# Optimization experiments

Measured on AMD Instinct MI355X. Metric: run time of the kernel, lower is better.

## Reference

```python
import jax, jax.numpy as jnp
import numpy as np

B, LQ, LK, H, DK, DV, E = 4, 1024, 1024, 12, 64, 768, 768
TOPK = 64
TEMP = 0.5
NEG = -10000.0


def setup_inputs() -> dict:
    key = jax.random.key(0)
    ks = jax.random.split(key, 10)
    s = 0.02  # weight init scale
    return {
        "q": jax.random.normal(ks[0], (B, LQ, E), jnp.float32),
        "k": jax.random.normal(ks[1], (B, LK, E), jnp.float32),
        "v": jax.random.normal(ks[2], (B, LK, DV), jnp.float32),
        "qpos": jnp.zeros((B, LQ), jnp.int32),
        "kpos": jnp.zeros((B, LK), jnp.int32),
        "qk_mask": jax.random.normal(ks[3], (B, 1, LQ, LK), jnp.float32) * 0.1,
        "k_mask": jax.random.normal(ks[4], (B, 1, LK, 1), jnp.float32) * 0.1,
        "post_softmax_mask": (jax.random.uniform(ks[5], (B, 1, LQ, LK)) > 0.1).astype(jnp.float32),
        "w_qs": jax.random.normal(ks[6], (E, H * DK), jnp.float32) * s,
        "w_ks": jax.random.normal(ks[7], (E, H * DK), jnp.float32) * s,
        "w_vs": jax.random.normal(ks[8], (DV, H * DV), jnp.float32) * s,
        "fc": jax.random.normal(ks[9], (H * DV, DV), jnp.float32) * s,
    }


def reference(q, k, v, qpos, kpos, qk_mask, k_mask, post_softmax_mask, w_qs, w_ks, w_vs, fc):
    residual = v
    # project and split heads: [b, len, h, d] -> [b, h, len, d]
    qh = (q @ w_qs).reshape(B, LQ, H, DK).transpose(0, 2, 1, 3)
    kh = (k @ w_ks).reshape(B, LK, H, DK).transpose(0, 2, 1, 3)
    vh = (v @ w_vs).reshape(B, LK, H, DV).transpose(0, 2, 1, 3)

    # scaled dot-product scores [b, h, lq, lk]
    attn = jnp.einsum('bhqd,bhkd->bhqk', qh / np.float32(np.sqrt(DK)), kh)
    attn = attn + qk_mask                              # additive qk mask
    attn = attn + jnp.squeeze(k_mask, -1)[:, :, None, :]  # additive key mask

    # topk sparsification: keep top-k scores, fill rest with -10000
    topk_vals, topk_idx = jax.lax.top_k(attn, TOPK)
    attn = jnp.put_along_axis(jnp.full_like(attn, NEG), topk_idx, topk_vals,
                              axis=-1, inplace=False)

    # temperature + stable softmax in fp32
    attn = attn / max(TEMP, 1e-6)
    attn = jax.nn.softmax(attn.astype(jnp.float32), axis=-1).astype(v.dtype)

    # post-softmax multiplicative mask + renorm (renorm_post_mask=True)
    attn = attn * post_softmax_mask
    attn = attn / jnp.maximum(attn.sum(axis=-1, keepdims=True), 1e-6)

    # straight-through argmax hardening (use_argmax=True)
    hard = jax.nn.one_hot(jnp.argmax(attn, axis=-1), LK, dtype=attn.dtype)
    attn = hard - jax.lax.stop_gradient(attn) + attn

    # attend, merge heads, output projection + residual (dropout=0)
    head_output = jnp.einsum('bhqk,bhkd->bhqd', attn, vh)
    output = head_output.transpose(0, 2, 1, 3).reshape(B, LQ, H * DV) @ fc
    output = output + residual
    return (output, attn)
```

## Files before the change

### kernel.cpp

```cpp
#include <hip/hip_runtime.h>

constexpr int NB  = 4;
constexpr int NH  = 12;
constexpr int SEQ = 1024;
constexpr int DKd = 64;
constexpr int DVd = 768;
constexpr int Ed  = 768;
constexpr int HVd = 9216;

typedef float f32x4 __attribute__((ext_vector_type(4)));
typedef short s16x8 __attribute__((ext_vector_type(8)));

__device__ __forceinline__ unsigned short f2bf(float f) {
  unsigned int u = __builtin_bit_cast(unsigned int, f);
  u += 0x7fffu + ((u >> 16) & 1u);
  return (unsigned short)(u >> 16);
}
__device__ __forceinline__ float bf2f(unsigned short h) {
  return __builtin_bit_cast(float, (unsigned int)h << 16);
}
__device__ __forceinline__ float bf2f_lo(unsigned int u) {
  return __builtin_bit_cast(float, u << 16);
}
__device__ __forceinline__ float bf2f_hi(unsigned int u) {
  return __builtin_bit_cast(float, u & 0xffff0000u);
}
__device__ __forceinline__ bool better(float va, int ia, float vb, int ib) {
  return va > vb || (va == vb && ia < ib);
}

__device__ __forceinline__ f32x4 mfma_bf16_16x16x32(s16x8 a, s16x8 b, f32x4 c) {
  asm("v_mfma_f32_16x16x32_bf16 %0, %1, %2, %0" : "+v"(c) : "v"(a), "v"(b));
  return c;
}

#define GLOAD16(g, l)                                                          \
  __builtin_amdgcn_global_load_lds(                                            \
      (const __attribute__((address_space(1))) unsigned int*)(g),              \
      (__attribute__((address_space(3))) unsigned int*)(l), 16, 0, 0)

__global__ __launch_bounds__(256)
void split_qk_kernel(const float* __restrict__ q, const float* __restrict__ k,
                     unsigned short* __restrict__ Qhi, unsigned short* __restrict__ Qlo,
                     unsigned short* __restrict__ Khi, unsigned short* __restrict__ Klo,
                     int n4) {
  const float* src = blockIdx.z ? k : q;
  unsigned short* hi = blockIdx.z ? Khi : Qhi;
  unsigned short* lo = blockIdx.z ? Klo : Qlo;
  int i = blockIdx.x * 256 + threadIdx.x;
  const int stride = gridDim.x * 256;
  for (; i < n4; i += stride) {
    const f32x4 x = *(const f32x4*)&src[(size_t)i * 4];
    unsigned short h[4], l[4];
#pragma unroll
    for (int c = 0; c < 4; c++) {
      h[c] = f2bf(x[c]);
      l[c] = f2bf(x[c] - bf2f(h[c]));
    }
    uint2 uh, ul;
    uh.x = (unsigned)h[0] | ((unsigned)h[1] << 16);
    uh.y = (unsigned)h[2] | ((unsigned)h[3] << 16);
    ul.x = (unsigned)l[0] | ((unsigned)l[1] << 16);
    ul.y = (unsigned)l[2] | ((unsigned)l[3] << 16);
    *(uint2*)&hi[(size_t)i * 4] = uh;
    *(uint2*)&lo[(size_t)i * 4] = ul;
  }
}

__global__ __launch_bounds__(256)
void split_wT_kernel(const float* __restrict__ w_qs, const float* __restrict__ w_ks,
                     unsigned short* __restrict__ WqThi, unsigned short* __restrict__ WqTlo,
                     unsigned short* __restrict__ WkThi, unsigned short* __restrict__ WkTlo) {
  __shared__ float Ts[64][68];
  const float* src = blockIdx.z ? w_ks : w_qs;
  unsigned short* hi = blockIdx.z ? WkThi : WqThi;
  unsigned short* lo = blockIdx.z ? WkTlo : WqTlo;
  const int e0 = blockIdx.x * 64, n0 = blockIdx.y * 64;
  const int tid = threadIdx.x;
  const int row = tid >> 2, cc = (tid & 3) * 16;
#pragma unroll
  for (int j = 0; j < 4; j++)
    *(f32x4*)&Ts[row][cc + 4 * j] = *(const f32x4*)&src[(size_t)(e0 + row) * 768 + n0 + cc + 4 * j];
  __syncthreads();
  const int r = tid >> 2, cs = (tid & 3) * 16;
  s16x8 ph[2], pl[2];
#pragma unroll
  for (int j = 0; j < 16; j++) {
    const float v = Ts[cs + j][r];
    const unsigned short h = f2bf(v);
    const unsigned short l = f2bf(v - bf2f(h));
    ph[j >> 3][j & 7] = (short)h;
    pl[j >> 3][j & 7] = (short)l;
  }
  const size_t ob = (size_t)(n0 + r) * 768 + e0 + cs;
  *(s16x8*)&hi[ob] = ph[0];
  *(s16x8*)&hi[ob + 8] = ph[1];
  *(s16x8*)&lo[ob] = pl[0];
  *(s16x8*)&lo[ob + 8] = pl[1];
}

__global__ __launch_bounds__(256)
void qkproj_mfma_kernel(const unsigned short* __restrict__ Qhi, const unsigned short* __restrict__ Qlo,
                        const unsigned short* __restrict__ Khi, const unsigned short* __restrict__ Klo,
                        const unsigned short* __restrict__ WqThi, const unsigned short* __restrict__ WqTlo,
                        const unsigned short* __restrict__ WkThi, const unsigned short* __restrict__ WkTlo,
                        float* __restrict__ qh, float* __restrict__ kh) {
  const unsigned short* Ahi = blockIdx.z ? Khi : Qhi;
  const unsigned short* Alo = blockIdx.z ? Klo : Qlo;
  const unsigned short* Bhi = blockIdx.z ? WkThi : WqThi;
  const unsigned short* Blo = blockIdx.z ? WkTlo : WqTlo;
  float* C = blockIdx.z ? kh : qh;
  __shared__ unsigned short AhiS[128 * 64], AloS[128 * 64];
  __shared__ unsigned short BhiS[64 * 64], BloS[64 * 64];
  const int tid = threadIdx.x;
  const int wid = tid >> 6, lane = tid & 63;
  const int m0 = blockIdx.x * 128, n0 = blockIdx.y * 64;
  const int wr = (wid >> 1) * 64, wc = (wid & 1) * 32;
  const int lm = lane & 15, lq = lane >> 4;
  const int srow = wid * 8 + (lane >> 3);
  const int scols = (((lane & 7) * 16) ^ ((srow & 7) << 4)) >> 1;
  const int ldst = wid * 512;
  const int xs = (lm & 7) << 3;

  const unsigned short* ahi0 = Ahi + (size_t)(m0 + srow) * 768 + scols;
  const unsigned short* alo0 = Alo + (size_t)(m0 + srow) * 768 + scols;
  const unsigned short* bhi0 = Bhi + (size_t)(n0 + srow) * 768 + scols;
  const unsigned short* blo0 = Blo + (size_t)(n0 + srow) * 768 + scols;

  f32x4 acc[4][2];
#pragma unroll
  for (int m = 0; m < 4; m++)
#pragma unroll
    for (int n = 0; n < 2; n++)
#pragma unroll
      for (int r = 0; r < 4; r++) acc[m][n][r] = 0.f;

  for (int k0 = 0; k0 < 768; k0 += 64) {
#pragma unroll
    for (int j = 0; j < 4; j++) {
      GLOAD16(ahi0 + (size_t)j * 32 * 768 + k0, &AhiS[j * 2048 + ldst]);
      GLOAD16(alo0 + (size_t)j * 32 * 768 + k0, &AloS[j * 2048 + ldst]);
    }
#pragma unroll
    for (int j = 0; j < 2; j++) {
      GLOAD16(bhi0 + (size_t)j * 32 * 768 + k0, &BhiS[j * 2048 + ldst]);
      GLOAD16(blo0 + (size_t)j * 32 * 768 + k0, &BloS[j * 2048 + ldst]);
    }
    __syncthreads();
#pragma unroll
    for (int ks = 0; ks < 2; ks++) {
      const int kc = (ks * 32 + lq * 8) ^ xs;
      s16x8 ah[4], al[4], bh[2], bl[2];
#pragma unroll
      for (int m = 0; m < 4; m++) {
        ah[m] = *(const s16x8*)&AhiS[(wr + m * 16 + lm) * 64 + kc];
        al[m] = *(const s16x8*)&AloS[(wr + m * 16 + lm) * 64 + kc];
      }
#pragma unroll
      for (int n = 0; n < 2; n++) {
        bh[n] = *(const s16x8*)&BhiS[(wc + n * 16 + lm) * 64 + kc];
        bl[n] = *(const s16x8*)&BloS[(wc + n * 16 + lm) * 64 + kc];
      }
#pragma unroll
      for (int m = 0; m < 4; m++)
#pragma unroll
        for (int n = 0; n < 2; n++) {
          acc[m][n] = mfma_bf16_16x16x32(ah[m], bh[n], acc[m][n]);
          acc[m][n] = mfma_bf16_16x16x32(al[m], bh[n], acc[m][n]);
          acc[m][n] = mfma_bf16_16x16x32(ah[m], bl[n], acc[m][n]);
        }
    }
    __syncthreads();
  }
  asm volatile("s_nop 7\n\ts_nop 7");
#pragma unroll
  for (int m = 0; m < 4; m++)
#pragma unroll
    for (int n = 0; n < 2; n++)
#pragma unroll
      for (int r = 0; r < 4; r++)
        C[(size_t)(m0 + wr + m * 16 + lq * 4 + r) * 768 + n0 + wc + n * 16 + lm] =
            acc[m][n][r];
}

__global__ __launch_bounds__(256)
void score_argmax_kernel(const float* __restrict__ qh, const float* __restrict__ kh,
                         const float* __restrict__ qkm, const float* __restrict__ km,
                         const float* __restrict__ pm, float4* __restrict__ partials) {
  __shared__ float msS[64][128];
  __shared__ float QsT[64][64];
  __shared__ float KsT[64][128];
  const int b  = blockIdx.z;
  const int q0 = blockIdx.y * 64;
  const int k0 = blockIdx.x * 128;
  const int tid = threadIdx.x;
  const int ty = tid >> 4, tx = tid & 15;

  {
    const int row = tid >> 2, cc = (tid & 3) * 32;
    const size_t base = (size_t)(b * SEQ + q0 + row) * SEQ + k0 + cc;
#pragma unroll
    for (int i = 0; i < 8; i++) {
      const f32x4 qv = *(const f32x4*)&qkm[base + 4 * i];
      const f32x4 pv = *(const f32x4*)&pm[base + 4 * i];
      const f32x4 kv = *(const f32x4*)&km[b * SEQ + k0 + cc + 4 * i];
      f32x4 o;
#pragma unroll
      for (int c = 0; c < 4; c++) o[c] = pv[c] > 0.f ? qv[c] + kv[c] : -3.0e38f;
      *(f32x4*)&msS[row][cc + 4 * i] = o;
    }
  }

  const int qr = tid >> 2, qdc = (tid & 3) * 16;
  const int kr = tid >> 1, kdc = (tid & 1) * 32;
  const float* qbase = qh + (size_t)(b * SEQ + q0 + qr) * Ed + qdc;
  const float* kbase = kh + (size_t)(b * SEQ + k0 + kr) * Ed + kdc;
  const int kg0 = k0 + tx * 8;

  for (int h = 0; h < NH; h++) {
    __syncthreads();
#pragma unroll
    for (int j = 0; j < 4; j++) {
      const f32x4 qv = *(const f32x4*)&qbase[h * 64 + 4 * j];
#pragma unroll
      for (int c = 0; c < 4; c++) QsT[qdc + 4 * j + c][qr] = qv[c];
    }
#pragma unroll
    for (int j = 0; j < 8; j++) {
      const f32x4 kv = *(const f32x4*)&kbase[h * 64 + 4 * j];
#pragma unroll
      for (int c = 0; c < 4; c++) KsT[kdc + 4 * j + c][kr] = kv[c];
    }
    __syncthreads();

    float acc[4][8];
#pragma unroll
    for (int i = 0; i < 4; i++)
#pragma unroll
      for (int j = 0; j < 8; j++) acc[i][j] = 0.f;

#pragma unroll 8
    for (int kk = 0; kk < 64; kk++) {
      const f32x4 qf  = *(const f32x4*)&QsT[kk][ty * 4];
      const f32x4 kf0 = *(const f32x4*)&KsT[kk][tx * 8];
      const f32x4 kf1 = *(const f32x4*)&KsT[kk][tx * 8 + 4];
#pragma unroll
      for (int i = 0; i < 4; i++)
#pragma unroll
        for (int j = 0; j < 4; j++) {
          acc[i][j]     += qf[i] * kf0[j];
          acc[i][j + 4] += qf[i] * kf1[j];
        }
    }

#pragma unroll
    for (int i = 0; i < 4; i++) {
      const int qg = q0 + ty * 4 + i;
      const f32x4 m0v = *(const f32x4*)&msS[ty * 4 + i][tx * 8];
      const f32x4 m1v = *(const f32x4*)&msS[ty * 4 + i][tx * 8 + 4];
      float v1 = -3.0e38f, v2 = -3.0e38f;
      int i1 = 0, i2 = 0;
#pragma unroll
      for (int j = 0; j < 8; j++) {
        const float s = acc[i][j] * 0.125f + (j < 4 ? m0v[j & 3] : m1v[j & 3]);
        const int idx = kg0 + j;
        if (better(s, idx, v1, i1)) { v2 = v1; i2 = i1; v1 = s; i1 = idx; }
        else if (better(s, idx, v2, i2)) { v2 = s; i2 = idx; }
      }
#pragma unroll
      for (int off = 1; off < 16; off <<= 1) {
        const float w1 = __shfl_xor(v1, off); const int j1 = __shfl_xor(i1, off);
        const float w2 = __shfl_xor(v2, off); const int j2 = __shfl_xor(i2, off);
        if (better(w1, j1, v1, i1)) {
          if (better(v1, i1, w2, j2)) { v2 = v1; i2 = i1; } else { v2 = w2; i2 = j2; }
          v1 = w1; i1 = j1;
        } else if (better(w1, j1, v2, i2)) { v2 = w1; i2 = j1; }
      }
      if (tx == 0)
        partials[(size_t)((b * NH + h) * SEQ + qg) * 8 + blockIdx.x] =
            make_float4(v1, __int_as_float(i1), v2, __int_as_float(i2));
    }
  }
}

__global__ __launch_bounds__(256)
void argmax_reduce_kernel(const float4* __restrict__ partials, int* __restrict__ kmaxp,
                          float4* __restrict__ aux) {
  const int t = blockIdx.x * 256 + threadIdx.x;
  if (t >= NB * NH * SEQ) return;
  const float4* p = partials + (size_t)t * 8;
  float v1 = -3.0e38f, v2 = -3.0e38f;
  int i1 = 0, i2 = 0;
#pragma unroll
  for (int i = 0; i < 8; i++) {
    const float w1 = p[i].x; const int j1 = __float_as_int(p[i].y);
    const float w2 = p[i].z; const int j2 = __float_as_int(p[i].w);
    if (better(w1, j1, v1, i1)) {
      if (better(v1, i1, w2, j2)) { v2 = v1; i2 = i1; } else { v2 = w2; i2 = j2; }
      v1 = w1; i1 = j1;
    } else if (better(w1, j1, v2, i2)) { v2 = w1; i2 = j1; }
  }
  kmaxp[t] = i1;
  aux[t] = make_float4(v1, __int_as_float(i1), v2, __int_as_float(i2));
}

__global__ __launch_bounds__(256)
void rescue_kernel(const float4* __restrict__ aux, const float* __restrict__ q,
                   const float* __restrict__ k, const float* __restrict__ w_qs,
                   const float* __restrict__ w_ks, const float* __restrict__ qkm,
                   const float* __restrict__ km, const float* __restrict__ pm,
                   int* __restrict__ kmaxp) {
  const int row = blockIdx.x * 4 + (threadIdx.x >> 6);
  const float4 a = aux[row];
  if (a.x - a.z > 5e-4f) return;
  const int i1 = __float_as_int(a.y), i2 = __float_as_int(a.w);
  if (i1 == i2) return;
  const int bh = row >> 10, qq = row & 1023;
  const int b = bh / NH, h = bh % NH;
  const int lane = threadIdx.x & 63;
  const float* qr = q + (size_t)(b * SEQ + qq) * Ed;
  const float* k1 = k + (size_t)(b * SEQ + i1) * Ed;
  const float* k2 = k + (size_t)(b * SEQ + i2) * Ed;
  const float* wq = w_qs + h * DKd + lane;
  const float* wk = w_ks + h * DKd + lane;
  float qd = 0.f, k1d = 0.f, k2d = 0.f;
#pragma unroll 4
  for (int e = 0; e < Ed; e++) {
    const float wqe = wq[(size_t)e * 768];
    const float wke = wk[(size_t)e * 768];
    qd  += qr[e] * wqe;
    k1d += k1[e] * wke;
    k2d += k2[e] * wke;
  }
  float s1 = qd * k1d, s2 = qd * k2d;
#pragma unroll
  for (int off = 1; off < 64; off <<= 1) {
    s1 += __shfl_xor(s1, off);
    s2 += __shfl_xor(s2, off);
  }
  const size_t m1 = (size_t)(b * SEQ + qq) * SEQ + i1;
  const size_t m2 = (size_t)(b * SEQ + qq) * SEQ + i2;
  s1 = s1 * 0.125f + (pm[m1] > 0.f ? qkm[m1] + km[b * SEQ + i1] : -3.0e38f);
  s2 = s2 * 0.125f + (pm[m2] > 0.f ? qkm[m2] + km[b * SEQ + i2] : -3.0e38f);
  if (lane == 0) kmaxp[row] = better(s1, i1, s2, i2) ? i1 : i2;
}

__global__ __launch_bounds__(256)
void cvt_bf16_kernel(const float* __restrict__ v, unsigned short* __restrict__ Vbf, int n4) {
  int i = blockIdx.x * 256 + threadIdx.x;
  const int stride = gridDim.x * 256;
  for (; i < n4; i += stride) {
    const f32x4 x = *(const f32x4*)&v[(size_t)i * 4];
    uint2 u;
    u.x = (unsigned)f2bf(x[0]) | ((unsigned)f2bf(x[1]) << 16);
    u.y = (unsigned)f2bf(x[2]) | ((unsigned)f2bf(x[3]) << 16);
    *(uint2*)&Vbf[(size_t)i * 4] = u;
  }
}

__global__ __launch_bounds__(256)
void wvfc_gemm_kernel(const float* __restrict__ wvs, const float* __restrict__ fcw,
                      unsigned short* __restrict__ MstbT) {
  __shared__ unsigned short As[128][72];
  __shared__ unsigned short Bs[128][72];
  const int tid = threadIdx.x;
  const int h = blockIdx.z;
  const int m0 = blockIdx.x * 128, n0 = blockIdx.y * 128;
  const int wid = tid >> 6, lane = tid & 63;
  const int wr = (wid >> 1) * 64, wc = (wid & 1) * 64;
  const int lm = lane & 15, lq = lane >> 4;
  const int ar = tid >> 1, acb = (tid & 1) * 32;
  const int br = tid >> 2, bnb = (tid & 3) * 32;

  f32x4 acc[4][4];
#pragma unroll
  for (int m = 0; m < 4; m++)
#pragma unroll
    for (int n = 0; n < 4; n++)
#pragma unroll
      for (int r = 0; r < 4; r++) acc[m][n][r] = 0.f;

  for (int k0 = 0; k0 < 768; k0 += 64) {
    const float* asrc = wvs + (size_t)(m0 + ar) * HVd + h * 768 + k0 + acb;
    const float* bsrc = fcw + (size_t)(h * 768 + k0 + br) * 768 + n0 + bnb;
    f32x4 a4[8], b4[8];
#pragma unroll
    for (int i = 0; i < 8; i++) a4[i] = *(const f32x4*)&asrc[4 * i];
#pragma unroll
    for (int i = 0; i < 8; i++) b4[i] = *(const f32x4*)&bsrc[4 * i];
    __syncthreads();
#pragma unroll
    for (int i = 0; i < 4; i++) {
      s16x8 pk;
#pragma unroll
      for (int j = 0; j < 8; j++) pk[j] = (short)f2bf(a4[2 * i + (j >> 2)][j & 3]);
      *(s16x8*)&As[ar][acb + 8 * i] = pk;
    }
#pragma unroll
    for (int i = 0; i < 8; i++)
#pragma unroll
      for (int c = 0; c < 4; c++) Bs[bnb + 4 * i + c][br] = f2bf(b4[i][c]);
    __syncthreads();
#pragma unroll
    for (int ks = 0; ks < 2; ks++) {
      s16x8 af[4], bfr[4];
#pragma unroll
      for (int m = 0; m < 4; m++)
        af[m] = *(const s16x8*)&As[wr + m * 16 + lm][ks * 32 + lq * 8];
#pragma unroll
      for (int n = 0; n < 4; n++)
        bfr[n] = *(const s16x8*)&Bs[wc + n * 16 + lm][ks * 32 + lq * 8];
#pragma unroll
      for (int m = 0; m < 4; m++)
#pragma unroll
        for (int n = 0; n < 4; n++)
          acc[m][n] = mfma_bf16_16x16x32(af[m], bfr[n], acc[m][n]);
    }
  }
  asm volatile("s_nop 7\n\ts_nop 7");
#pragma unroll
  for (int m = 0; m < 4; m++)
#pragma unroll
    for (int n = 0; n < 4; n++) {
      const int grow0 = m0 + wr + m * 16 + lq * 4;
      const int gcol  = n0 + wc + n * 16 + lm;
      uint2 u;
      u.x = (unsigned)f2bf(acc[m][n][0]) | ((unsigned)f2bf(acc[m][n][1]) << 16);
      u.y = (unsigned)f2bf(acc[m][n][2]) | ((unsigned)f2bf(acc[m][n][3]) << 16);
      *(uint2*)&MstbT[(size_t)(h * 768 + gcol) * 768 + grow0] = u;
    }
}

__global__ __launch_bounds__(256)
void ugemm_kernel(const unsigned short* __restrict__ Vbf,
                  const unsigned short* __restrict__ MstbT,
                  unsigned short* __restrict__ U, int h0) {
  __shared__ unsigned short As[128 * 64];
  __shared__ unsigned short Bs[128 * 64];
  const int tid = threadIdx.x;
  const int h = h0 + blockIdx.z;
  const int bx = (int)blockIdx.x;
  const int sx = ((bx & 7) << 2) | (bx >> 3);
  const int m0 = sx * 128, n0 = blockIdx.y * 128;
  const int wid = tid >> 6, lane = tid & 63;
  const int wr = (wid >> 1) * 64, wc = (wid & 1) * 64;
  const int lm = lane & 15, lq = lane >> 4;
  const int srow = tid >> 3, scol = (tid & 7) * 8;
  const int ldst = (tid >> 6) * 512;

  const unsigned short* asrc = Vbf + (size_t)(m0 + srow) * 768 + scol;
  const unsigned short* bsrc = MstbT + (size_t)(h * 768 + n0 + srow) * 768 + scol;

  f32x4 acc[4][4];
#pragma unroll
  for (int m = 0; m < 4; m++)
#pragma unroll
    for (int n = 0; n < 4; n++)
#pragma unroll
      for (int r = 0; r < 4; r++) acc[m][n][r] = 0.f;

  for (int k0 = 0; k0 < 768; k0 += 64) {
#pragma unroll
    for (int j = 0; j < 4; j++)
      GLOAD16(asrc + (size_t)j * 32 * 768 + k0, &As[j * 2048 + ldst]);
#pragma unroll
    for (int j = 0; j < 4; j++)
      GLOAD16(bsrc + (size_t)j * 32 * 768 + k0, &Bs[j * 2048 + ldst]);
    __syncthreads();
#pragma unroll
    for (int ks = 0; ks < 2; ks++) {
      s16x8 af[4], bfr[4];
#pragma unroll
      for (int m = 0; m < 4; m++)
        af[m] = *(const s16x8*)&As[(wr + m * 16 + lm) * 64 + ks * 32 + lq * 8];
#pragma unroll
      for (int n = 0; n < 4; n++)
        bfr[n] = *(const s16x8*)&Bs[(wc + n * 16 + lm) * 64 + ks * 32 + lq * 8];
#pragma unroll
      for (int m = 0; m < 4; m++)
#pragma unroll
        for (int n = 0; n < 4; n++)
          acc[m][n] = mfma_bf16_16x16x32(af[m], bfr[n], acc[m][n]);
    }
    __syncthreads();
  }
  asm volatile("s_nop 7\n\ts_nop 7");
  const size_t urow0 = (size_t)blockIdx.z * 4096;
#pragma unroll
  for (int m = 0; m < 4; m++)
#pragma unroll
    for (int r = 0; r < 4; r++) {
      const int row = m0 + wr + m * 16 + lq * 4 + r;
      uint2 u;
      u.x = (unsigned)f2bf(acc[m][0][r]) | ((unsigned)f2bf(acc[m][1][r]) << 16);
      u.y = (unsigned)f2bf(acc[m][2][r]) | ((unsigned)f2bf(acc[m][3][r]) << 16);
      *(uint2*)&U[(urow0 + row) * 768 + n0 + wc + lm * 4] = u;
    }
}

__global__ __launch_bounds__(192)
void gathersum_kernel(const unsigned short* __restrict__ U, const int* __restrict__ kmaxp,
                      const float* __restrict__ v, float* __restrict__ out0,
                      int h0, int nhg) {
  const int row = blockIdx.x;
  const int b = row >> 10, q = row & 1023;
  const int t = threadIdx.x;
  float a0 = 0.f, a1 = 0.f, a2 = 0.f, a3 = 0.f;
  for (int hg = 0; hg < nhg; hg++) {
    const int g = kmaxp[((b * NH + h0 + hg) << 10) + q];
    const uint2 u = *(const uint2*)&U[((size_t)hg * 4096 + (b << 10) + g) * 768 + t * 4];
    a0 += bf2f_lo(u.x);
    a1 += bf2f_hi(u.x);
    a2 += bf2f_lo(u.y);
    a3 += bf2f_hi(u.y);
  }
  const int chunk = t >> 4, lmm = t & 15;
  const size_t ob = (size_t)row * 768 + chunk * 64 + lmm;
  if (h0 == 0) {
    out0[ob +  0] = a0 + v[ob +  0];
    out0[ob + 16] = a1 + v[ob + 16];
    out0[ob + 32] = a2 + v[ob + 32];
    out0[ob + 48] = a3 + v[ob + 48];
  } else {
    out0[ob +  0] += a0;
    out0[ob + 16] += a1;
    out0[ob + 32] += a2;
    out0[ob + 48] += a3;
  }
}

__global__ void onehot_kernel(const int* __restrict__ kmaxp, f32x4* __restrict__ attn, int n4) {
  int i = blockIdx.x * blockDim.x + threadIdx.x;
  const int stride = gridDim.x * blockDim.x;
  for (; i < n4; i += stride) {
    const int row = i >> 8;
    const int c0 = (i & 255) * 4;
    const int km = kmaxp[row];
    f32x4 o;
#pragma unroll
    for (int c = 0; c < 4; c++) o[c] = (c0 + c == km) ? 1.0f : 0.0f;
    attn[i] = o;
  }
}

extern "C" void kernel_launch(void* const* d_in, const int* in_sizes, int n_in,
                              void* d_out, int out_size, void* d_ws, size_t ws_size,
                              hipStream_t stream) {
  (void)in_sizes; (void)n_in; (void)out_size;
  const float* q       = (const float*)d_in[0];
  const float* k       = (const float*)d_in[1];
  const float* v       = (const float*)d_in[2];
  const float* qk_mask = (const float*)d_in[5];
  const float* k_mask  = (const float*)d_in[6];
  const float* pmask   = (const float*)d_in[7];
  const float* w_qs    = (const float*)d_in[8];
  const float* w_ks    = (const float*)d_in[9];
  const float* w_vs    = (const float*)d_in[10];
  const float* fc      = (const float*)d_in[11];

  float* out0 = (float*)d_out;
  float* attn = out0 + (size_t)NB * SEQ * DVd;

  char* ws = (char*)d_ws;
  unsigned short* Qhi   = (unsigned short*)ws;
  unsigned short* Qlo   = (unsigned short*)(ws + 6291456);
  unsigned short* WqThi = (unsigned short*)(ws + 12582912);
  unsigned short* WqTlo = (unsigned short*)(ws + 13762560);
  unsigned short* WkThi = (unsigned short*)(ws + 14942208);
  unsigned short* WkTlo = (unsigned short*)(ws + 16121856);
  int* kmaxp            = (int*)(ws + 20447232);
  unsigned short* Khi   = (unsigned short*)(ws + 20643840);
  unsigned short* Klo   = (unsigned short*)(ws + 26935296);
  float* qh             = (float*)(ws + 33226752);
  float* kh             = (float*)(ws + 45809664);
  float4* partials      = (float4*)ws;
  float4* aux           = (float4*)(ws + 6291456);
  unsigned short* MstbT = (unsigned short*)ws;
  unsigned short* Vbf   = (unsigned short*)(ws + 14155776);
  unsigned short* U     = (unsigned short*)(ws + 20643840);

  const bool big = ws_size >= (size_t)96141312;

  split_qk_kernel<<<dim3(1536, 1, 2), 256, 0, stream>>>(q, k, Qhi, Qlo, Khi, Klo,
                                                        NB * SEQ * Ed / 4);
  split_wT_kernel<<<dim3(12, 12, 2), 256, 0, stream>>>(w_qs, w_ks, WqThi, WqTlo,
                                                       WkThi, WkTlo);

  qkproj_mfma_kernel<<<dim3(32, 12, 2), 256, 0, stream>>>(
      Qhi, Qlo, Khi, Klo, WqThi, WqTlo, WkThi, WkTlo, qh, kh);

  score_argmax_kernel<<<dim3(8, 16, NB), 256, 0, stream>>>(qh, kh, qk_mask, k_mask,
                                                           pmask, partials);
  argmax_reduce_kernel<<<dim3(192), 256, 0, stream>>>(partials, kmaxp, aux);

  rescue_kernel<<<dim3(12288), 256, 0, stream>>>(aux, q, k, w_qs, w_ks,
                                                 qk_mask, k_mask, pmask, kmaxp);

  cvt_bf16_kernel<<<dim3(3072), 256, 0, stream>>>(v, Vbf, NB * SEQ * DVd / 4);
  wvfc_gemm_kernel<<<dim3(6, 6, NH), 256, 0, stream>>>(w_vs, fc, MstbT);

  if (big) {
    ugemm_kernel<<<dim3(32, 6, 12), 256, 0, stream>>>(Vbf, MstbT, U, 0);
    gathersum_kernel<<<dim3(NB * SEQ), 192, 0, stream>>>(U, kmaxp, v, out0, 0, 12);
  } else {
    ugemm_kernel<<<dim3(32, 6, 6), 256, 0, stream>>>(Vbf, MstbT, U, 0);
    gathersum_kernel<<<dim3(NB * SEQ), 192, 0, stream>>>(U, kmaxp, v, out0, 0, 6);
    ugemm_kernel<<<dim3(32, 6, 6), 256, 0, stream>>>(Vbf, MstbT, U, 6);
    gathersum_kernel<<<dim3(NB * SEQ), 192, 0, stream>>>(U, kmaxp, v, out0, 6, 6);
  }

  onehot_kernel<<<dim3(2048), 256, 0, stream>>>(kmaxp, (f32x4*)attn,
                                                (int)((size_t)NB * NH * SEQ * SEQ / 4));
}
```

Baseline: 500.3 us.

## Compute attention scores with split-bf16 MFMA per head instead of FP32 FMA

```diff
diff --git a/kernel.cpp b/kernel.cpp
--- a/kernel.cpp
+++ b/kernel.cpp
@@ -184,88 +184,110 @@
 }
 
 __global__ __launch_bounds__(256)
-void score_argmax_kernel(const float* __restrict__ qh, const float* __restrict__ kh,
-                         const float* __restrict__ qkm, const float* __restrict__ km,
-                         const float* __restrict__ pm, float4* __restrict__ partials) {
-  __shared__ float msS[64][128];
-  __shared__ float QsT[64][64];
-  __shared__ float KsT[64][128];
-  const int b  = blockIdx.z;
-  const int q0 = blockIdx.y * 64;
-  const int k0 = blockIdx.x * 128;
+void score_mfma2_kernel(const float* __restrict__ qh, const float* __restrict__ kh,
+                        const float* __restrict__ qkm, const float* __restrict__ km,
+                        const float* __restrict__ pm, float4* __restrict__ partials) {
+  __shared__ unsigned short QhS[128][72], QlS[128][72];
+  __shared__ unsigned short KhS[128][72], KlS[128][72];
+  const int bh = blockIdx.z, b = bh / NH, h = bh % NH;
+  const int q0 = blockIdx.y * 128, k0 = blockIdx.x * 128;
   const int tid = threadIdx.x;
-  const int ty = tid >> 4, tx = tid & 15;
-
-  {
-    const int row = tid >> 2, cc = (tid & 3) * 32;
-    const size_t base = (size_t)(b * SEQ + q0 + row) * SEQ + k0 + cc;
-#pragma unroll
-    for (int i = 0; i < 8; i++) {
-      const f32x4 qv = *(const f32x4*)&qkm[base + 4 * i];
-      const f32x4 pv = *(const f32x4*)&pm[base + 4 * i];
-      const f32x4 kv = *(const f32x4*)&km[b * SEQ + k0 + cc + 4 * i];
-      f32x4 o;
-#pragma unroll
-      for (int c = 0; c < 4; c++) o[c] = pv[c] > 0.f ? qv[c] + kv[c] : -3.0e38f;
-      *(f32x4*)&msS[row][cc + 4 * i] = o;
-    }
-  }
-
-  const int qr = tid >> 2, qdc = (tid & 3) * 16;
-  const int kr = tid >> 1, kdc = (tid & 1) * 32;
-  const float* qbase = qh + (size_t)(b * SEQ + q0 + qr) * Ed + qdc;
-  const float* kbase = kh + (size_t)(b * SEQ + k0 + kr) * Ed + kdc;
-  const int kg0 = k0 + tx * 8;
-
-  for (int h = 0; h < NH; h++) {
-    __syncthreads();
-#pragma unroll
-    for (int j = 0; j < 4; j++) {
-      const f32x4 qv = *(const f32x4*)&qbase[h * 64 + 4 * j];
-#pragma unroll
-      for (int c = 0; c < 4; c++) QsT[qdc + 4 * j + c][qr] = qv[c];
-    }
-#pragma unroll
-    for (int j = 0; j < 8; j++) {
-      const f32x4 kv = *(const f32x4*)&kbase[h * 64 + 4 * j];
-#pragma unroll
-      for (int c = 0; c < 4; c++) KsT[kdc + 4 * j + c][kr] = kv[c];
-    }
-    __syncthreads();
-
-    float acc[4][8];
-#pragma unroll
-    for (int i = 0; i < 4; i++)
-#pragma unroll
-      for (int j = 0; j < 8; j++) acc[i][j] = 0.f;
-
-#pragma unroll 8
-    for (int kk = 0; kk < 64; kk++) {
-      const f32x4 qf  = *(const f32x4*)&QsT[kk][ty * 4];
-      const f32x4 kf0 = *(const f32x4*)&KsT[kk][tx * 8];
-      const f32x4 kf1 = *(const f32x4*)&KsT[kk][tx * 8 + 4];
-#pragma unroll
-      for (int i = 0; i < 4; i++)
-#pragma unroll
-        for (int j = 0; j < 4; j++) {
-          acc[i][j]     += qf[i] * kf0[j];
-          acc[i][j + 4] += qf[i] * kf1[j];
-        }
-    }
-
-#pragma unroll
-    for (int i = 0; i < 4; i++) {
-      const int qg = q0 + ty * 4 + i;
-      const f32x4 m0v = *(const f32x4*)&msS[ty * 4 + i][tx * 8];
-      const f32x4 m1v = *(const f32x4*)&msS[ty * 4 + i][tx * 8 + 4];
+  const int wid = tid >> 6, lane = tid & 63;
+  const int wr = (wid >> 1) * 64, wc = (wid & 1) * 64;
+  const int lm = lane & 15, lq = lane >> 4;
+  const int srow = tid >> 1, scb = (tid & 1) * 32;
+
+  const float* qsrc = qh + (size_t)(b * SEQ + q0 + srow) * 768 + h * 64 + scb;
+  const float* ksrc = kh + (size_t)(b * SEQ + k0 + srow) * 768 + h * 64 + scb;
+#pragma unroll
+  for (int i = 0; i < 4; i++) {
+    const f32x4 x0 = *(const f32x4*)&qsrc[8 * i];
+    const f32x4 x1 = *(const f32x4*)&qsrc[8 * i + 4];
+    s16x8 hi8, lo8;
+#pragma unroll
+    for (int c = 0; c < 4; c++) {
+      const unsigned short h0 = f2bf(x0[c]);
+      hi8[c] = (short)h0;
+      lo8[c] = (short)f2bf(x0[c] - bf2f(h0));
+      const unsigned short h1 = f2bf(x1[c]);
+      hi8[4 + c] = (short)h1;
+      lo8[4 + c] = (short)f2bf(x1[c] - bf2f(h1));
+    }
+    *(s16x8*)&QhS[srow][scb + 8 * i] = hi8;
+    *(s16x8*)&QlS[srow][scb + 8 * i] = lo8;
+  }
+#pragma unroll
+  for (int i = 0; i < 4; i++) {
+    const f32x4 x0 = *(const f32x4*)&ksrc[8 * i];
+    const f32x4 x1 = *(const f32x4*)&ksrc[8 * i + 4];
+    s16x8 hi8, lo8;
+#pragma unroll
+    for (int c = 0; c < 4; c++) {
+      const unsigned short h0 = f2bf(x0[c]);
+      hi8[c] = (short)h0;
+      lo8[c] = (short)f2bf(x0[c] - bf2f(h0));
+      const unsigned short h1 = f2bf(x1[c]);
+      hi8[4 + c] = (short)h1;
+      lo8[4 + c] = (short)f2bf(x1[c] - bf2f(h1));
+    }
+    *(s16x8*)&KhS[srow][scb + 8 * i] = hi8;
+    *(s16x8*)&KlS[srow][scb + 8 * i] = lo8;
+  }
+  __syncthreads();
+
+  f32x4 acc[4][4];
+#pragma unroll
+  for (int m = 0; m < 4; m++)
+#pragma unroll
+    for (int n = 0; n < 4; n++)
+#pragma unroll
+      for (int r = 0; r < 4; r++) acc[m][n][r] = 0.f;
+
+#pragma unroll
+  for (int ks = 0; ks < 2; ks++) {
+    const int kc = ks * 32 + lq * 8;
+    s16x8 ah[4], al[4], bh4[4], bl4[4];
+#pragma unroll
+    for (int m = 0; m < 4; m++) {
+      ah[m] = *(const s16x8*)&QhS[wr + m * 16 + lm][kc];
+      al[m] = *(const s16x8*)&QlS[wr + m * 16 + lm][kc];
+    }
+#pragma unroll
+    for (int n = 0; n < 4; n++) {
+      bh4[n] = *(const s16x8*)&KhS[wc + n * 16 + lm][kc];
+      bl4[n] = *(const s16x8*)&KlS[wc + n * 16 + lm][kc];
+    }
+#pragma unroll
+    for (int m = 0; m < 4; m++)
+#pragma unroll
+      for (int n = 0; n < 4; n++) {
+        acc[m][n] = mfma_bf16_16x16x32(ah[m], bh4[n], acc[m][n]);
+        acc[m][n] = mfma_bf16_16x16x32(al[m], bh4[n], acc[m][n]);
+        acc[m][n] = mfma_bf16_16x16x32(ah[m], bl4[n], acc[m][n]);
+      }
+  }
+  asm volatile("s_nop 7\n\ts_nop 7");
+
+  float kmv[4];
+#pragma unroll
+  for (int n = 0; n < 4; n++) kmv[n] = km[b * SEQ + k0 + wc + n * 16 + lm];
+
+#pragma unroll
+  for (int m = 0; m < 4; m++)
+#pragma unroll
+    for (int r = 0; r < 4; r++) {
+      const int qg = q0 + wr + m * 16 + lq * 4 + r;
+      const size_t mrow = (size_t)(b * SEQ + qg) * SEQ + k0 + wc;
       float v1 = -3.0e38f, v2 = -3.0e38f;
       int i1 = 0, i2 = 0;
 #pragma unroll
-      for (int j = 0; j < 8; j++) {
-        const float s = acc[i][j] * 0.125f + (j < 4 ? m0v[j & 3] : m1v[j & 3]);
-        const int idx = kg0 + j;
-        if (better(s, idx, v1, i1)) { v2 = v1; i2 = i1; v1 = s; i1 = idx; }
-        else if (better(s, idx, v2, i2)) { v2 = s; i2 = idx; }
+      for (int n = 0; n < 4; n++) {
+        const int kg = k0 + wc + n * 16 + lm;
+        const float pv = pm[mrow + n * 16 + lm];
+        const float qm = qkm[mrow + n * 16 + lm];
+        const float s = pv > 0.f ? acc[m][n][r] * 0.125f + qm + kmv[n] : -3.0e38f;
+        if (better(s, kg, v1, i1)) { v2 = v1; i2 = i1; v1 = s; i1 = kg; }
+        else if (better(s, kg, v2, i2)) { v2 = s; i2 = kg; }
       }
 #pragma unroll
       for (int off = 1; off < 16; off <<= 1) {
@@ -276,11 +298,10 @@
           v1 = w1; i1 = j1;
         } else if (better(w1, j1, v2, i2)) { v2 = w1; i2 = j1; }
       }
-      if (tx == 0)
-        partials[(size_t)((b * NH + h) * SEQ + qg) * 8 + blockIdx.x] =
+      if (lm == 0)
+        partials[(size_t)(bh * SEQ + qg) * 16 + blockIdx.x * 2 + (wid & 1)] =
             make_float4(v1, __int_as_float(i1), v2, __int_as_float(i2));
     }
-  }
 }
 
 __global__ __launch_bounds__(256)
@@ -288,11 +309,11 @@
                           float4* __restrict__ aux) {
   const int t = blockIdx.x * 256 + threadIdx.x;
   if (t >= NB * NH * SEQ) return;
-  const float4* p = partials + (size_t)t * 8;
+  const float4* p = partials + (size_t)t * 16;
   float v1 = -3.0e38f, v2 = -3.0e38f;
   int i1 = 0, i2 = 0;
 #pragma unroll
-  for (int i = 0; i < 8; i++) {
+  for (int i = 0; i < 16; i++) {
     const float w1 = p[i].x; const int j1 = __float_as_int(p[i].y);
     const float w2 = p[i].z; const int j2 = __float_as_int(p[i].w);
     if (better(w1, j1, v1, i1)) {
@@ -312,7 +333,7 @@
                    int* __restrict__ kmaxp) {
   const int row = blockIdx.x * 4 + (threadIdx.x >> 6);
   const float4 a = aux[row];
-  if (a.x - a.z > 5e-4f) return;
+  if (a.x - a.z > 2e-3f) return;
   const int i1 = __float_as_int(a.y), i2 = __float_as_int(a.w);
   if (i1 == i2) return;
   const int bh = row >> 10, qq = row & 1023;
@@ -546,7 +567,7 @@
 extern "C" void kernel_launch(void* const* d_in, const int* in_sizes, int n_in,
                               void* d_out, int out_size, void* d_ws, size_t ws_size,
                               hipStream_t stream) {
-  (void)in_sizes; (void)n_in; (void)out_size;
+  (void)in_sizes; (void)n_in; (void)out_size; (void)ws_size;
   const float* q       = (const float*)d_in[0];
   const float* k       = (const float*)d_in[1];
   const float* v       = (const float*)d_in[2];
@@ -564,22 +585,20 @@
   char* ws = (char*)d_ws;
   unsigned short* Qhi   = (unsigned short*)ws;
   unsigned short* Qlo   = (unsigned short*)(ws + 6291456);
-  unsigned short* WqThi = (unsigned short*)(ws + 12582912);
-  unsigned short* WqTlo = (unsigned short*)(ws + 13762560);
-  unsigned short* WkThi = (unsigned short*)(ws + 14942208);
-  unsigned short* WkTlo = (unsigned short*)(ws + 16121856);
-  int* kmaxp            = (int*)(ws + 20447232);
-  unsigned short* Khi   = (unsigned short*)(ws + 20643840);
-  unsigned short* Klo   = (unsigned short*)(ws + 26935296);
+  unsigned short* Khi   = (unsigned short*)(ws + 12582912);
+  unsigned short* Klo   = (unsigned short*)(ws + 18874368);
+  unsigned short* WqThi = (unsigned short*)(ws + 25165824);
+  unsigned short* WqTlo = (unsigned short*)(ws + 26345472);
+  unsigned short* WkThi = (unsigned short*)(ws + 27525120);
+  unsigned short* WkTlo = (unsigned short*)(ws + 28704768);
   float* qh             = (float*)(ws + 33226752);
   float* kh             = (float*)(ws + 45809664);
   float4* partials      = (float4*)ws;
-  float4* aux           = (float4*)(ws + 6291456);
+  float4* aux           = (float4*)(ws + 12582912);
   unsigned short* MstbT = (unsigned short*)ws;
   unsigned short* Vbf   = (unsigned short*)(ws + 14155776);
-  unsigned short* U     = (unsigned short*)(ws + 20643840);
-
-  const bool big = ws_size >= (size_t)96141312;
+  unsigned short* U     = (unsigned short*)(ws + 20447232);
+  int* kmaxp            = (int*)(ws + 58195968);
 
   split_qk_kernel<<<dim3(1536, 1, 2), 256, 0, stream>>>(q, k, Qhi, Qlo, Khi, Klo,
                                                         NB * SEQ * Ed / 4);
@@ -589,8 +608,8 @@
   qkproj_mfma_kernel<<<dim3(32, 12, 2), 256, 0, stream>>>(
       Qhi, Qlo, Khi, Klo, WqThi, WqTlo, WkThi, WkTlo, qh, kh);
 
-  score_argmax_kernel<<<dim3(8, 16, NB), 256, 0, stream>>>(qh, kh, qk_mask, k_mask,
-                                                           pmask, partials);
+  score_mfma2_kernel<<<dim3(8, 8, NB * NH), 256, 0, stream>>>(
+      qh, kh, qk_mask, k_mask, pmask, partials);
   argmax_reduce_kernel<<<dim3(192), 256, 0, stream>>>(partials, kmaxp, aux);
 
   rescue_kernel<<<dim3(12288), 256, 0, stream>>>(aux, q, k, w_qs, w_ks,
@@ -599,15 +618,10 @@
   cvt_bf16_kernel<<<dim3(3072), 256, 0, stream>>>(v, Vbf, NB * SEQ * DVd / 4);
   wvfc_gemm_kernel<<<dim3(6, 6, NH), 256, 0, stream>>>(w_vs, fc, MstbT);
 
-  if (big) {
-    ugemm_kernel<<<dim3(32, 6, 12), 256, 0, stream>>>(Vbf, MstbT, U, 0);
-    gathersum_kernel<<<dim3(NB * SEQ), 192, 0, stream>>>(U, kmaxp, v, out0, 0, 12);
-  } else {
-    ugemm_kernel<<<dim3(32, 6, 6), 256, 0, stream>>>(Vbf, MstbT, U, 0);
-    gathersum_kernel<<<dim3(NB * SEQ), 192, 0, stream>>>(U, kmaxp, v, out0, 0, 6);
-    ugemm_kernel<<<dim3(32, 6, 6), 256, 0, stream>>>(Vbf, MstbT, U, 6);
-    gathersum_kernel<<<dim3(NB * SEQ), 192, 0, stream>>>(U, kmaxp, v, out0, 6, 6);
-  }
+  ugemm_kernel<<<dim3(32, 6, 6), 256, 0, stream>>>(Vbf, MstbT, U, 0);
+  gathersum_kernel<<<dim3(NB * SEQ), 192, 0, stream>>>(U, kmaxp, v, out0, 0, 6);
+  ugemm_kernel<<<dim3(32, 6, 6), 256, 0, stream>>>(Vbf, MstbT, U, 6);
+  gathersum_kernel<<<dim3(NB * SEQ), 192, 0, stream>>>(U, kmaxp, v, out0, 6, 6);
 
   onehot_kernel<<<dim3(2048), 256, 0, stream>>>(kmaxp, (f32x4*)attn,
                                                 (int)((size_t)NB * NH * SEQ * SEQ / 4));
```

New measurement: 625.0 us. +24.9%, slower.
